# Performance work log

Measured on AMD Instinct MI355X. Metric: run time of the kernel, lower is better.

The kernel has to match this reference:

```python
import jax, jax.numpy as jnp
import numpy as np

N = 50000   # nodes
E = 800000  # edges (avg degree 16)
G = 64      # graphs in batch


def setup_inputs() -> dict:
    key = jax.random.key(0)
    ks = jax.random.split(key, 32)
    w = lambda k, shape, s=0.05: (jax.random.normal(k, shape, jnp.float32) * s)
    inp = {}
    inp["x"] = jax.random.normal(ks[0], (N, 3), jnp.float32)
    inp["edge_index"] = jax.random.randint(ks[1], (2, E), 0, N)
    inp["batch"] = jnp.sort(jax.random.randint(ks[2], (N,), 0, G))
    # TransformerConv 1: in=3, heads=2, d=32 -> out 64 (concat)
    inp["Wq1"] = w(ks[3], (3, 64));  inp["bq1"] = w(ks[4], (64,))
    inp["Wk1"] = w(ks[5], (3, 64));  inp["bk1"] = w(ks[6], (64,))
    inp["Wv1"] = w(ks[7], (3, 64));  inp["bv1"] = w(ks[8], (64,))
    inp["Ws1"] = w(ks[9], (3, 64));  inp["bs1"] = w(ks[10], (64,))
    # TransformerConv 2: in=64, heads=2, d=64 -> out 128 (concat)
    inp["Wq2"] = w(ks[11], (64, 128)); inp["bq2"] = w(ks[12], (128,))
    inp["Wk2"] = w(ks[13], (64, 128)); inp["bk2"] = w(ks[14], (128,))
    inp["Wv2"] = w(ks[15], (64, 128)); inp["bv2"] = w(ks[16], (128,))
    inp["Ws2"] = w(ks[17], (64, 128)); inp["bs2"] = w(ks[18], (128,))
    # MLP head
    inp["W1"] = w(ks[19], (128, 32)); inp["b1"] = w(ks[20], (32,))
    inp["W2"] = w(ks[21], (32, 128)); inp["b2"] = w(ks[22], (128,))
    inp["W3"] = w(ks[23], (128, 40)); inp["b3"] = w(ks[24], (40,))
    return inp


def _transformer_conv(x, src, dst, Wq, bq, Wk, bk, Wv, bv, Ws, bs, H, d):
    """PyG TransformerConv (concat=True, root_weight=True, beta=False)."""
    n = x.shape[0]
    q = (x @ Wq + bq).reshape(n, H, d)
    k = (x @ Wk + bk).reshape(n, H, d)
    v = (x @ Wv + bv).reshape(n, H, d)
    # per-edge attention logits: q_i . k_j / sqrt(d), i=dst, j=src  -> [E, H]
    s = (q[dst] * k[src]).sum(-1) / jnp.sqrt(jnp.float32(d))
    # segment softmax over edges grouped by destination node
    m = jax.ops.segment_max(s, dst, num_segments=n)
    m = jnp.where(jnp.isfinite(m), m, 0.0)
    e = jnp.exp(s - m[dst])
    denom = jax.ops.segment_sum(e, dst, num_segments=n)
    alpha = e / jnp.maximum(denom[dst], 1e-16)
    # scatter-add weighted values
    out = jax.ops.segment_sum(alpha[:, :, None] * v[src], dst, num_segments=n)
    return out.reshape(n, H * d) + x @ Ws + bs  # skip connection


def reference(x, edge_index, batch,
              Wq1, bq1, Wk1, bk1, Wv1, bv1, Ws1, bs1,
              Wq2, bq2, Wk2, bk2, Wv2, bv2, Ws2, bs2,
              W1, b1, W2, b2, W3, b3):
    src, dst = edge_index[0], edge_index[1]
    h = jax.nn.relu(_transformer_conv(x, src, dst, Wq1, bq1, Wk1, bk1,
                                      Wv1, bv1, Ws1, bs1, 2, 32))
    h = jax.nn.relu(_transformer_conv(h, src, dst, Wq2, bq2, Wk2, bk2,
                                      Wv2, bv2, Ws2, bs2, 2, 64))
    # global max pool over graphs
    p = jax.ops.segment_max(h, batch, num_segments=G)
    p = jnp.where(jnp.isfinite(p), p, 0.0)
    x_latent = jax.nn.relu(p @ W1 + b1)
    y = jax.nn.relu(x_latent @ W2 + b2)
    return (y @ W3 + b3, x_latent)
```

## Files before the change

### kernel.cpp

```cpp
#include <hip/hip_runtime.h>
#include <hip/hip_bf16.h>

typedef short s16x8 __attribute__((ext_vector_type(8)));
typedef float f32x4 __attribute__((ext_vector_type(4)));

#define LOG2E 1.4426950408889634f

__device__ __forceinline__ float bfl(unsigned w) { return __uint_as_float(w << 16); }
__device__ __forceinline__ float bfh(unsigned w) { return __uint_as_float(w & 0xffff0000u); }
__device__ __forceinline__ unsigned f2bf(float f) {
    unsigned u = __float_as_uint(f);
    return (u + 0x7fffu + ((u >> 16) & 1u)) >> 16;
}

__global__ void deg_kernel(const int* __restrict__ dst, int* __restrict__ deg, int E) {
    int e = blockIdx.x * blockDim.x + threadIdx.x;
    if (e < E) atomicAdd(&deg[dst[e]], 1);
}

__global__ void scan_reduce(const int* __restrict__ deg, int* __restrict__ bsum, int n) {
    __shared__ int sh[256];
    int t = threadIdx.x;
    int i = blockIdx.x * 256 + t;
    sh[t] = (i < n) ? deg[i] : 0;
    __syncthreads();
    for (int s = 128; s > 0; s >>= 1) {
        if (t < s) sh[t] += sh[t + s];
        __syncthreads();
    }
    if (t == 0) bsum[blockIdx.x] = sh[0];
}

__global__ void scan_blocks(const int* __restrict__ bsum, int* __restrict__ boff,
                            int nb, int* __restrict__ off, int n) {
    __shared__ int sh[256];
    int t = threadIdx.x;
    int v = (t < nb) ? bsum[t] : 0;
    sh[t] = v;
    __syncthreads();
    for (int d = 1; d < 256; d <<= 1) {
        int x = (t >= d) ? sh[t - d] : 0;
        __syncthreads();
        sh[t] += x;
        __syncthreads();
    }
    if (t < nb) boff[t] = sh[t] - v;
    if (t == 255) off[n] = sh[255];
}

__global__ void scan_apply(const int* __restrict__ deg, const int* __restrict__ boff,
                           int* __restrict__ off, int* __restrict__ cursor, int n) {
    __shared__ int sh[256];
    int t = threadIdx.x;
    int i = blockIdx.x * 256 + t;
    int v = (i < n) ? deg[i] : 0;
    sh[t] = v;
    __syncthreads();
    for (int d = 1; d < 256; d <<= 1) {
        int x = (t >= d) ? sh[t - d] : 0;
        __syncthreads();
        sh[t] += x;
        __syncthreads();
    }
    int ex = sh[t] - v + boff[blockIdx.x];
    if (i < n) {
        off[i] = ex;
        cursor[i] = ex;
    }
}

__global__ void scatter_kernel(const int* __restrict__ src, const int* __restrict__ dst,
                               int* __restrict__ cursor, int* __restrict__ srcs, int E) {
    int e = blockIdx.x * blockDim.x + threadIdx.x;
    if (e < E) {
        int p = atomicAdd(&cursor[dst[e]], 1);
        srcs[p] = src[e];
    }
}

__global__ void prep_all(const float* __restrict__ Wq1, const float* __restrict__ bq1,
                         const float* __restrict__ Wk1,
                         const float* __restrict__ Wq2, const float* __restrict__ bq2,
                         const float* __restrict__ Wk2,
                         const float* __restrict__ Wv2, const float* __restrict__ Ws2,
                         float* __restrict__ c1, float* __restrict__ wcat,
                         ushort* __restrict__ bfragY, ushort* __restrict__ B192,
                         int* __restrict__ deg, unsigned* __restrict__ pool,
                         int n, int nbdeg, int poolsz) {
    int b = blockIdx.x, t = threadIdx.x;
    if (b == 0) {
        if (t < 18) {
            int h = t / 9, rr = t % 9, r = rr / 3, rp = rr % 3;
            float s = 0.f;
            for (int d = 0; d < 32; ++d)
                s += Wq1[r * 64 + h * 32 + d] * Wk1[rp * 64 + h * 32 + d];
            c1[t] = s;
        } else if (t < 24) {
            int u = t - 18, h = u / 3, rp = u % 3;
            float s = 0.f;
            for (int d = 0; d < 32; ++d)
                s += bq1[h * 32 + d] * Wk1[rp * 64 + h * 32 + d];
            c1[t] = s;
        } else if (t >= 64 && t < 192) {
            int cc = t - 64, h = cc >> 6, kp = cc & 63;
            float s = 0.f;
            for (int d = 0; d < 64; ++d)
                s += bq2[h * 64 + d] * Wk2[kp * 128 + h * 64 + d];
            wcat[cc] = s;
        }
    } else if (b < 33) {
        int idx = (b - 1) * 256 + t;
        int k = idx >> 7, cc = idx & 127, h = cc >> 6, kp = cc & 63;
        float s = 0.f;
        for (int d = 0; d < 64; ++d)
            s += Wq2[k * 128 + h * 64 + d] * Wk2[kp * 128 + h * 64 + d];
        int frag = ((cc >> 4) << 1) | (k >> 5);
        int l = (cc & 15) | (((k >> 3) & 3) << 4);
        bfragY[(size_t)frag * 512 + l * 8 + (k & 7)] = (ushort)f2bf(s);
    } else if (b < 45) {
        int tt = (b - 33) * 256 + t;
        int frag = tt >> 6, l = tt & 63;
        int ct = frag / 6, ks = frag % 6;
        int c = ct * 16 + (l & 15);
        int kbase = ks * 32 + ((l >> 4) << 3);
#pragma unroll
        for (int e = 0; e < 8; ++e) {
            int k = kbase + e;
            float v;
            if (k < 64) v = (c < 64) ? Wv2[k * 128 + c] : 0.f;
            else if (k < 128) v = (c >= 64) ? Wv2[(k - 64) * 128 + c] : 0.f;
            else v = Ws2[(k - 128) * 128 + c];
            B192[(size_t)frag * 512 + l * 8 + e] = (ushort)f2bf(v);
        }
    } else if (b < 45 + nbdeg) {
        int i = (b - 45) * 256 + t;
        if (i < n) deg[i] = 0;
    } else {
        int i = (b - 45 - nbdeg) * 256 + t;
        if (i < poolsz) pool[i] = 0;
    }
}

__global__ __launch_bounds__(256) void attn1f(
        const float* __restrict__ x, const float* __restrict__ c1,
        const float* __restrict__ Wv, const float* __restrict__ bv,
        const float* __restrict__ Ws, const float* __restrict__ bs,
        const int* __restrict__ off, const int* __restrict__ srcs,
        unsigned* __restrict__ h1b, int n) {
    int lane = threadIdx.x & 63;
    int g = lane >> 3, sl = lane & 7;
    int i = (blockIdx.x * (blockDim.x >> 6) + (threadIdx.x >> 6)) * 8 + g;
    bool act = i < n;
    int ic = act ? i : 0;
    float x0 = x[ic * 3], x1 = x[ic * 3 + 1], x2 = x[ic * 3 + 2];
    float y0[3], y1[3];
#pragma unroll
    for (int rp = 0; rp < 3; ++rp) {
        y0[rp] = x0 * c1[rp] + x1 * c1[3 + rp] + x2 * c1[6 + rp] + c1[18 + rp];
        y1[rp] = x0 * c1[9 + rp] + x1 * c1[12 + rp] + x2 * c1[15 + rp] + c1[21 + rp];
    }
    const float SC = 0.17677669529663688f * LOG2E;
    int e0 = act ? off[ic] : 0, e1 = act ? off[ic + 1] : 0;
    float d0 = 0.f, d1 = 0.f;
    float a0x = 0.f, a0y = 0.f, a0z = 0.f, a1x = 0.f, a1y = 0.f, a1z = 0.f;
    for (int e = e0 + sl; e < e1; e += 8) {
        int j = srcs[e];
        float xj0 = x[j * 3], xj1 = x[j * 3 + 1], xj2 = x[j * 3 + 2];
        float p0 = exp2f((y0[0] * xj0 + y0[1] * xj1 + y0[2] * xj2) * SC);
        float p1 = exp2f((y1[0] * xj0 + y1[1] * xj1 + y1[2] * xj2) * SC);
        d0 += p0; a0x += p0 * xj0; a0y += p0 * xj1; a0z += p0 * xj2;
        d1 += p1; a1x += p1 * xj0; a1y += p1 * xj1; a1z += p1 * xj2;
    }
#pragma unroll
    for (int mask = 1; mask <= 4; mask <<= 1) {
        d0 += __shfl_xor(d0, mask); d1 += __shfl_xor(d1, mask);
        a0x += __shfl_xor(a0x, mask); a0y += __shfl_xor(a0y, mask);
        a0z += __shfl_xor(a0z, mask); a1x += __shfl_xor(a1x, mask);
        a1y += __shfl_xor(a1y, mask); a1z += __shfl_xor(a1z, mask);
    }
    if (!act) return;
    int head = sl >> 2;
    float dh = head ? d1 : d0;
    float inv = 1.f / fmaxf(dh, 1e-16f);
    float sg = dh > 0.f ? 1.f : 0.f;
    float Ax = (head ? a1x : a0x) * inv;
    float Ay = (head ? a1y : a0y) * inv;
    float Az = (head ? a1z : a0z) * inv;
    unsigned pk[4];
#pragma unroll
    for (int u = 0; u < 4; ++u) {
        int c = sl * 8 + 2 * u;
        float2 wv0 = *(const float2*)&Wv[c], wv1 = *(const float2*)&Wv[64 + c],
               wv2 = *(const float2*)&Wv[128 + c];
        float2 ws0 = *(const float2*)&Ws[c], ws1 = *(const float2*)&Ws[64 + c],
               ws2 = *(const float2*)&Ws[128 + c];
        float2 bbv = *(const float2*)&bv[c];
        float2 bbs = *(const float2*)&bs[c];
        float v0 = Ax * wv0.x + Ay * wv1.x + Az * wv2.x + sg * bbv.x +
                   x0 * ws0.x + x1 * ws1.x + x2 * ws2.x + bbs.x;
        float v1 = Ax * wv0.y + Ay * wv1.y + Az * wv2.y + sg * bbv.y +
                   x0 * ws0.y + x1 * ws1.y + x2 * ws2.y + bbs.y;
        pk[u] = f2bf(fmaxf(v0, 0.f)) | (f2bf(fmaxf(v1, 0.f)) << 16);
    }
    uint4 pa = {pk[0], pk[1], pk[2], pk[3]};
    *(uint4*)&h1b[(size_t)i * 32 + sl * 4] = pa;
}

__global__ __launch_bounds__(256) void lin2Y(const ushort* __restrict__ h1b,
                                             const ushort* __restrict__ bfragY,
                                             const float* __restrict__ wcat,
                                             float* __restrict__ Yp, int n) {
    int node0 = blockIdx.x * 16;
    int w = threadIdx.x >> 6, l = threadIdx.x & 63;
    int arow = node0 + (l & 15);
    if (arow >= n) arow = n - 1;
    s16x8 a0 = *(const s16x8*)&h1b[(size_t)arow * 64 + ((l >> 4) << 3)];
    s16x8 a1 = *(const s16x8*)&h1b[(size_t)arow * 64 + 32 + ((l >> 4) << 3)];
    int cl = l & 15;
#pragma unroll
    for (int qq = 0; qq < 2; ++qq) {
        int ct = w * 2 + qq;
        s16x8 b0 = *(const s16x8*)&bfragY[(size_t)(ct * 2 + 0) * 512 + l * 8];
        s16x8 b1 = *(const s16x8*)&bfragY[(size_t)(ct * 2 + 1) * 512 + l * 8];
        f32x4 acc = {0.f, 0.f, 0.f, 0.f};
        acc = __builtin_amdgcn_mfma_f32_16x16x32_bf16(a0, b0, acc, 0, 0, 0);
        acc = __builtin_amdgcn_mfma_f32_16x16x32_bf16(a1, b1, acc, 0, 0, 0);
        int cg = ct * 16 + cl;
        float bb = wcat[cg];
#pragma unroll
        for (int r = 0; r < 4; ++r) {
            int node = node0 + ((l >> 4) << 2) + r;
            if (node < n) Yp[(size_t)node * 128 + cg] = acc[r] + bb;
        }
    }
}

__global__ void attn2_kernel(const float* __restrict__ Yp, const unsigned* __restrict__ h1u,
                             const int* __restrict__ off, const int* __restrict__ srcs,
                             unsigned* __restrict__ a01, float2* __restrict__ sig2, int n) {
    int i = blockIdx.x * (blockDim.x >> 6) + (threadIdx.x >> 6);
    int lane = threadIdx.x & 63;
    if (i >= n) return;
    int og = lane >> 3, sl = lane & 7;
    int e0 = off[i], e1 = off[i + 1];
    const float SC = 0.125f * LOG2E;
    float4 ya0 = *(const float4*)&Yp[(size_t)i * 128 + 8 * sl];
    float4 ya1 = *(const float4*)&Yp[(size_t)i * 128 + 8 * sl + 4];
    float4 yb0 = *(const float4*)&Yp[(size_t)i * 128 + 64 + 8 * sl];
    float4 yb1 = *(const float4*)&Yp[(size_t)i * 128 + 64 + 8 * sl + 4];
    float d0 = 0.f, d1 = 0.f;
    float a0[8] = {0.f, 0.f, 0.f, 0.f, 0.f, 0.f, 0.f, 0.f};
    float a1[8] = {0.f, 0.f, 0.f, 0.f, 0.f, 0.f, 0.f, 0.f};
    for (int e = e0 + og; e < e1; e += 8) {
        int j = srcs[e];
        uint4 hb = *(const uint4*)&h1u[(size_t)j * 32 + 4 * sl];
        float h[8];
        h[0] = bfl(hb.x); h[1] = bfh(hb.x); h[2] = bfl(hb.y); h[3] = bfh(hb.y);
        h[4] = bfl(hb.z); h[5] = bfh(hb.z); h[6] = bfl(hb.w); h[7] = bfh(hb.w);
        float t0 = ya0.x * h[0] + ya0.y * h[1] + ya0.z * h[2] + ya0.w * h[3] +
                   ya1.x * h[4] + ya1.y * h[5] + ya1.z * h[6] + ya1.w * h[7];
        float t1 = yb0.x * h[0] + yb0.y * h[1] + yb0.z * h[2] + yb0.w * h[3] +
                   yb1.x * h[4] + yb1.y * h[5] + yb1.z * h[6] + yb1.w * h[7];
        t0 += __shfl_xor(t0, 1); t0 += __shfl_xor(t0, 2); t0 += __shfl_xor(t0, 4);
        t1 += __shfl_xor(t1, 1); t1 += __shfl_xor(t1, 2); t1 += __shfl_xor(t1, 4);
        float p0 = exp2f(t0 * SC);
        float p1 = exp2f(t1 * SC);
        d0 += p0;
        d1 += p1;
#pragma unroll
        for (int k = 0; k < 8; ++k) {
            a0[k] += p0 * h[k];
            a1[k] += p1 * h[k];
        }
    }
#pragma unroll
    for (int mask = 8; mask <= 32; mask <<= 1) {
        d0 += __shfl_xor(d0, mask);
        d1 += __shfl_xor(d1, mask);
#pragma unroll
        for (int k = 0; k < 8; ++k) {
            a0[k] += __shfl_xor(a0[k], mask);
            a1[k] += __shfl_xor(a1[k], mask);
        }
    }
    if (og == 0) {
        float i0 = 1.f / fmaxf(d0, 1e-16f), i1 = 1.f / fmaxf(d1, 1e-16f);
        uint4 pa, pb;
        pa.x = f2bf(a0[0] * i0) | (f2bf(a0[1] * i0) << 16);
        pa.y = f2bf(a0[2] * i0) | (f2bf(a0[3] * i0) << 16);
        pa.z = f2bf(a0[4] * i0) | (f2bf(a0[5] * i0) << 16);
        pa.w = f2bf(a0[6] * i0) | (f2bf(a0[7] * i0) << 16);
        pb.x = f2bf(a1[0] * i1) | (f2bf(a1[1] * i1) << 16);
        pb.y = f2bf(a1[2] * i1) | (f2bf(a1[3] * i1) << 16);
        pb.z = f2bf(a1[4] * i1) | (f2bf(a1[5] * i1) << 16);
        pb.w = f2bf(a1[6] * i1) | (f2bf(a1[7] * i1) << 16);
        *(uint4*)&a01[(size_t)i * 64 + 4 * sl] = pa;
        *(uint4*)&a01[(size_t)i * 64 + 32 + 4 * sl] = pb;
        if (sl == 0) {
            float2 sg = {d0 > 0.f ? 1.f : 0.f, d1 > 0.f ? 1.f : 0.f};
            sig2[i] = sg;
        }
    }
}

__global__ __launch_bounds__(256) void epi2(
        const ushort* __restrict__ a01, const ushort* __restrict__ h1b,
        const ushort* __restrict__ B192, const float* __restrict__ bv,
        const float* __restrict__ bs, const float* __restrict__ sig2,
        const int* __restrict__ batch, unsigned* __restrict__ pool, int n) {
    __shared__ float po[16][128];
    __shared__ int pg[16];
    int node0 = blockIdx.x * 16;
    int w = threadIdx.x >> 6, l = threadIdx.x & 63;
    int arow = node0 + (l & 15);
    int arc = (arow < n) ? arow : (n - 1);
    int koff = (l >> 4) << 3;
    s16x8 af[6];
    af[0] = *(const s16x8*)&a01[(size_t)arc * 128 + 0 + koff];
    af[1] = *(const s16x8*)&a01[(size_t)arc * 128 + 32 + koff];
    af[2] = *(const s16x8*)&a01[(size_t)arc * 128 + 64 + koff];
    af[3] = *(const s16x8*)&a01[(size_t)arc * 128 + 96 + koff];
    af[4] = *(const s16x8*)&h1b[(size_t)arc * 64 + 0 + koff];
    af[5] = *(const s16x8*)&h1b[(size_t)arc * 64 + 32 + koff];
    if (threadIdx.x < 16)
        pg[threadIdx.x] = (node0 + threadIdx.x < n) ? batch[node0 + threadIdx.x] : -1;
    int cl = l & 15;
#pragma unroll
    for (int qq = 0; qq < 2; ++qq) {
        int ct = w * 2 + qq;
        f32x4 acc = {0.f, 0.f, 0.f, 0.f};
#pragma unroll
        for (int ks = 0; ks < 6; ++ks) {
            s16x8 b = *(const s16x8*)&B192[(size_t)(ct * 6 + ks) * 512 + l * 8];
            acc = __builtin_amdgcn_mfma_f32_16x16x32_bf16(af[ks], b, acc, 0, 0, 0);
        }
        int cg = ct * 16 + cl;
        int head = cg >> 6;
        float bbs = bs[cg], bbv = bv[cg];
#pragma unroll
        for (int r = 0; r < 4; ++r) {
            int row = ((l >> 4) << 2) + r;
            int node = node0 + row;
            float sg = (node < n) ? sig2[node * 2 + head] : 0.f;
            po[row][cg] = fmaxf(acc[r] + sg * bbv + bbs, 0.f);
        }
    }
    __syncthreads();
    int t = threadIdx.x;
    if (t < 128) {
        int curg = -1;
        float mx = 0.f;
        for (int r = 0; r < 16; ++r) {
            int g = pg[r];
            if (g < 0) continue;
            if (g != curg) {
                if (curg >= 0) atomicMax(&pool[(size_t)curg * 128 + t], __float_as_uint(mx));
                curg = g;
                mx = 0.f;
            }
            mx = fmaxf(mx, po[r][t]);
        }
        if (curg >= 0) atomicMax(&pool[(size_t)curg * 128 + t], __float_as_uint(mx));
    }
}

__global__ void head_kernel(const unsigned* __restrict__ pbits,
                            const float* __restrict__ W1, const float* __restrict__ b1,
                            const float* __restrict__ W2, const float* __restrict__ b2,
                            const float* __restrict__ W3, const float* __restrict__ b3,
                            float* __restrict__ out, int G) {
    int g = blockIdx.x;
    int t = threadIdx.x;
    __shared__ float ps[128], xl[32], y[128];
    ps[t] = __uint_as_float(pbits[g * 128 + t]);
    __syncthreads();
    if (t < 32) {
        float a = b1[t];
        for (int k = 0; k < 128; ++k) a += ps[k] * W1[k * 32 + t];
        a = fmaxf(a, 0.f);
        xl[t] = a;
        out[G * 40 + g * 32 + t] = a;
    }
    __syncthreads();
    {
        float a = b2[t];
        for (int k = 0; k < 32; ++k) a += xl[k] * W2[k * 128 + t];
        y[t] = fmaxf(a, 0.f);
    }
    __syncthreads();
    if (t < 40) {
        float a = b3[t];
        for (int k = 0; k < 128; ++k) a += y[k] * W3[k * 40 + t];
        out[g * 40 + t] = a;
    }
}

extern "C" void kernel_launch(void* const* d_in, const int* in_sizes, int n_in,
                              void* d_out, int out_size, void* d_ws, size_t ws_size,
                              hipStream_t stream) {
    const float* x = (const float*)d_in[0];
    const int* eidx = (const int*)d_in[1];
    const int* batch = (const int*)d_in[2];
    const float *Wq1 = (const float*)d_in[3], *bq1 = (const float*)d_in[4];
    const float *Wk1 = (const float*)d_in[5], *bk1 = (const float*)d_in[6];
    const float *Wv1 = (const float*)d_in[7], *bv1 = (const float*)d_in[8];
    const float *Ws1 = (const float*)d_in[9], *bs1 = (const float*)d_in[10];
    const float *Wq2 = (const float*)d_in[11], *bq2 = (const float*)d_in[12];
    const float *Wk2 = (const float*)d_in[13], *bk2 = (const float*)d_in[14];
    const float *Wv2 = (const float*)d_in[15], *bv2 = (const float*)d_in[16];
    const float *Ws2 = (const float*)d_in[17], *bs2 = (const float*)d_in[18];
    const float *W1 = (const float*)d_in[19], *b1 = (const float*)d_in[20];
    const float *W2 = (const float*)d_in[21], *b2 = (const float*)d_in[22];
    const float *W3 = (const float*)d_in[23], *b3 = (const float*)d_in[24];
    (void)bk1; (void)bk2;

    const int N = in_sizes[0] / 3;
    const int E = in_sizes[1] / 2;
    const int G = out_size / 72;
    const int* esrc = eidx;
    const int* edst = eidx + E;
    const int NB = (N + 255) / 256;
    const int POOLSZ = G * 128;
    const int PB = (POOLSZ + 255) / 256;

    char* w = (char*)d_ws;
    size_t o = 0;
    auto alloc = [&](size_t bytes) {
        void* p = w + o;
        o = (o + bytes + 255) & ~(size_t)255;
        return p;
    };
    float* c1buf = (float*)alloc(24 * 4);
    float* wcat = (float*)alloc(128 * 4);
    ushort* bfragY = (ushort*)alloc(16 * 512 * 2);
    ushort* B192 = (ushort*)alloc(48 * 512 * 2);
    unsigned* h1b = (unsigned*)alloc((size_t)N * 32 * 4);
    float* Yp = (float*)alloc((size_t)N * 128 * 4);
    unsigned* a01 = (unsigned*)alloc((size_t)N * 64 * 4);
    float* sig2 = (float*)alloc((size_t)N * 2 * 4);
    int* deg = (int*)alloc((size_t)N * 4);
    int* off = (int*)alloc((size_t)(N + 1) * 4);
    int* cursor = (int*)alloc((size_t)N * 4);
    int* srcs = (int*)alloc((size_t)E * 4);
    unsigned* pool = (unsigned*)alloc((size_t)POOLSZ * 4);
    int* bsum = (int*)alloc(256 * 4);
    int* boff = (int*)alloc(256 * 4);
    (void)ws_size;

    prep_all<<<45 + NB + PB, 256, 0, stream>>>(Wq1, bq1, Wk1, Wq2, bq2, Wk2, Wv2, Ws2,
                                               c1buf, wcat, bfragY, B192, deg, pool,
                                               N, NB, POOLSZ);

    deg_kernel<<<(E + 255) / 256, 256, 0, stream>>>(edst, deg, E);
    scan_reduce<<<NB, 256, 0, stream>>>(deg, bsum, N);
    scan_blocks<<<1, 256, 0, stream>>>(bsum, boff, NB, off, N);
    scan_apply<<<NB, 256, 0, stream>>>(deg, boff, off, cursor, N);
    scatter_kernel<<<(E + 255) / 256, 256, 0, stream>>>(esrc, edst, cursor, srcs, E);

    attn1f<<<(N + 31) / 32, 256, 0, stream>>>(x, c1buf, Wv1, bv1, Ws1, bs1, off, srcs,
                                              h1b, N);

    lin2Y<<<(N + 15) / 16, 256, 0, stream>>>((const ushort*)h1b, bfragY, wcat, Yp, N);
    attn2_kernel<<<(N + 3) / 4, 256, 0, stream>>>(Yp, h1b, off, srcs, a01,
                                                  (float2*)sig2, N);
    epi2<<<(N + 15) / 16, 256, 0, stream>>>((const ushort*)a01, (const ushort*)h1b, B192,
                                            bv2, bs2, sig2, batch, pool, N);

    head_kernel<<<G, 128, 0, stream>>>(pool, W1, b1, W2, b2, W3, b3, (float*)d_out, G);
}
```

Baseline: 193.8 us.

## Split layer-2 attention into score kernel and weighted-aggregation kernel

Splits the fused layer-2 attention kernel in two. The first kernel computes per-edge exponentiated scores and writes them to a new E-sized float2 buffer. The second kernel aggregates, with one wave per node and one feature per lane, looping over edges serially. This removes the 16-accumulator register pressure and the cross-lane reduction tree, but adds an extra kernel launch, a full E*8-byte write and re-read, and a second gather of h1 rows with a serial per-edge loop.

```diff
diff --git a/kernel.cpp b/kernel.cpp
--- a/kernel.cpp
+++ b/kernel.cpp
@@ -8,6 +8,7 @@
 
 __device__ __forceinline__ float bfl(unsigned w) { return __uint_as_float(w << 16); }
 __device__ __forceinline__ float bfh(unsigned w) { return __uint_as_float(w & 0xffff0000u); }
+__device__ __forceinline__ float ubf(ushort u) { return __uint_as_float((unsigned)u << 16); }
 __device__ __forceinline__ unsigned f2bf(float f) {
     unsigned u = __float_as_uint(f);
     return (u + 0x7fffu + ((u >> 16) & 1u)) >> 16;
@@ -235,9 +236,10 @@
     }
 }
 
-__global__ void attn2_kernel(const float* __restrict__ Yp, const unsigned* __restrict__ h1u,
-                             const int* __restrict__ off, const int* __restrict__ srcs,
-                             unsigned* __restrict__ a01, float2* __restrict__ sig2, int n) {
+__global__ __launch_bounds__(256) void attn2s(
+        const float* __restrict__ Yp, const unsigned* __restrict__ h1u,
+        const int* __restrict__ off, const int* __restrict__ srcs,
+        float2* __restrict__ pbuf, int n) {
     int i = blockIdx.x * (blockDim.x >> 6) + (threadIdx.x >> 6);
     int lane = threadIdx.x & 63;
     if (i >= n) return;
@@ -248,58 +250,46 @@
     float4 ya1 = *(const float4*)&Yp[(size_t)i * 128 + 8 * sl + 4];
     float4 yb0 = *(const float4*)&Yp[(size_t)i * 128 + 64 + 8 * sl];
     float4 yb1 = *(const float4*)&Yp[(size_t)i * 128 + 64 + 8 * sl + 4];
-    float d0 = 0.f, d1 = 0.f;
-    float a0[8] = {0.f, 0.f, 0.f, 0.f, 0.f, 0.f, 0.f, 0.f};
-    float a1[8] = {0.f, 0.f, 0.f, 0.f, 0.f, 0.f, 0.f, 0.f};
     for (int e = e0 + og; e < e1; e += 8) {
         int j = srcs[e];
         uint4 hb = *(const uint4*)&h1u[(size_t)j * 32 + 4 * sl];
-        float h[8];
-        h[0] = bfl(hb.x); h[1] = bfh(hb.x); h[2] = bfl(hb.y); h[3] = bfh(hb.y);
-        h[4] = bfl(hb.z); h[5] = bfh(hb.z); h[6] = bfl(hb.w); h[7] = bfh(hb.w);
-        float t0 = ya0.x * h[0] + ya0.y * h[1] + ya0.z * h[2] + ya0.w * h[3] +
-                   ya1.x * h[4] + ya1.y * h[5] + ya1.z * h[6] + ya1.w * h[7];
-        float t1 = yb0.x * h[0] + yb0.y * h[1] + yb0.z * h[2] + yb0.w * h[3] +
-                   yb1.x * h[4] + yb1.y * h[5] + yb1.z * h[6] + yb1.w * h[7];
+        float t0 = ya0.x * bfl(hb.x) + ya0.y * bfh(hb.x) + ya0.z * bfl(hb.y) +
+                   ya0.w * bfh(hb.y) + ya1.x * bfl(hb.z) + ya1.y * bfh(hb.z) +
+                   ya1.z * bfl(hb.w) + ya1.w * bfh(hb.w);
+        float t1 = yb0.x * bfl(hb.x) + yb0.y * bfh(hb.x) + yb0.z * bfl(hb.y) +
+                   yb0.w * bfh(hb.y) + yb1.x * bfl(hb.z) + yb1.y * bfh(hb.z) +
+                   yb1.z * bfl(hb.w) + yb1.w * bfh(hb.w);
         t0 += __shfl_xor(t0, 1); t0 += __shfl_xor(t0, 2); t0 += __shfl_xor(t0, 4);
         t1 += __shfl_xor(t1, 1); t1 += __shfl_xor(t1, 2); t1 += __shfl_xor(t1, 4);
-        float p0 = exp2f(t0 * SC);
-        float p1 = exp2f(t1 * SC);
-        d0 += p0;
-        d1 += p1;
-#pragma unroll
-        for (int k = 0; k < 8; ++k) {
-            a0[k] += p0 * h[k];
-            a1[k] += p1 * h[k];
-        }
-    }
-#pragma unroll
-    for (int mask = 8; mask <= 32; mask <<= 1) {
-        d0 += __shfl_xor(d0, mask);
-        d1 += __shfl_xor(d1, mask);
-#pragma unroll
-        for (int k = 0; k < 8; ++k) {
-            a0[k] += __shfl_xor(a0[k], mask);
-            a1[k] += __shfl_xor(a1[k], mask);
-        }
-    }
-    if (og == 0) {
-        float i0 = 1.f / fmaxf(d0, 1e-16f), i1 = 1.f / fmaxf(d1, 1e-16f);
-        uint4 pa, pb;
-        pa.x = f2bf(a0[0] * i0) | (f2bf(a0[1] * i0) << 16);
-        pa.y = f2bf(a0[2] * i0) | (f2bf(a0[3] * i0) << 16);
-        pa.z = f2bf(a0[4] * i0) | (f2bf(a0[5] * i0) << 16);
-        pa.w = f2bf(a0[6] * i0) | (f2bf(a0[7] * i0) << 16);
-        pb.x = f2bf(a1[0] * i1) | (f2bf(a1[1] * i1) << 16);
-        pb.y = f2bf(a1[2] * i1) | (f2bf(a1[3] * i1) << 16);
-        pb.z = f2bf(a1[4] * i1) | (f2bf(a1[5] * i1) << 16);
-        pb.w = f2bf(a1[6] * i1) | (f2bf(a1[7] * i1) << 16);
-        *(uint4*)&a01[(size_t)i * 64 + 4 * sl] = pa;
-        *(uint4*)&a01[(size_t)i * 64 + 32 + 4 * sl] = pb;
         if (sl == 0) {
-            float2 sg = {d0 > 0.f ? 1.f : 0.f, d1 > 0.f ? 1.f : 0.f};
-            sig2[i] = sg;
-        }
+            float2 p = {exp2f(t0 * SC), exp2f(t1 * SC)};
+            pbuf[e] = p;
+        }
+    }
+}
+
+__global__ __launch_bounds__(256) void attn2pv(
+        const ushort* __restrict__ h1w, const int* __restrict__ off,
+        const int* __restrict__ srcs, const float2* __restrict__ pbuf,
+        ushort* __restrict__ a01, float2* __restrict__ sig2, int n) {
+    int i = blockIdx.x * (blockDim.x >> 6) + (threadIdx.x >> 6);
+    int lane = threadIdx.x & 63;
+    if (i >= n) return;
+    int e0 = off[i], e1 = off[i + 1];
+    float a0 = 0.f, a1 = 0.f, d0 = 0.f, d1 = 0.f;
+    for (int e = e0; e < e1; ++e) {
+        int j = srcs[e];
+        float2 p = pbuf[e];
+        float h = ubf(h1w[(size_t)j * 64 + lane]);
+        a0 += p.x * h; a1 += p.y * h;
+        d0 += p.x; d1 += p.y;
+    }
+    float i0 = 1.f / fmaxf(d0, 1e-16f), i1 = 1.f / fmaxf(d1, 1e-16f);
+    a01[(size_t)i * 128 + lane] = (ushort)f2bf(a0 * i0);
+    a01[(size_t)i * 128 + 64 + lane] = (ushort)f2bf(a1 * i1);
+    if (lane == 0) {
+        float2 sg = {d0 > 0.f ? 1.f : 0.f, d1 > 0.f ? 1.f : 0.f};
+        sig2[i] = sg;
     }
 }
 
@@ -436,8 +426,9 @@
     ushort* B192 = (ushort*)alloc(48 * 512 * 2);
     unsigned* h1b = (unsigned*)alloc((size_t)N * 32 * 4);
     float* Yp = (float*)alloc((size_t)N * 128 * 4);
-    unsigned* a01 = (unsigned*)alloc((size_t)N * 64 * 4);
+    ushort* a01 = (ushort*)alloc((size_t)N * 128 * 2);
     float* sig2 = (float*)alloc((size_t)N * 2 * 4);
+    float2* pbuf = (float2*)alloc((size_t)E * 8);
     int* deg = (int*)alloc((size_t)N * 4);
     int* off = (int*)alloc((size_t)(N + 1) * 4);
     int* cursor = (int*)alloc((size_t)N * 4);
@@ -461,9 +452,10 @@
                                               h1b, N);
 
     lin2Y<<<(N + 15) / 16, 256, 0, stream>>>((const ushort*)h1b, bfragY, wcat, Yp, N);
-    attn2_kernel<<<(N + 3) / 4, 256, 0, stream>>>(Yp, h1b, off, srcs, a01,
-                                                  (float2*)sig2, N);
-    epi2<<<(N + 15) / 16, 256, 0, stream>>>((const ushort*)a01, (const ushort*)h1b, B192,
+    attn2s<<<(N + 3) / 4, 256, 0, stream>>>(Yp, h1b, off, srcs, pbuf, N);
+    attn2pv<<<(N + 3) / 4, 256, 0, stream>>>((const ushort*)h1b, off, srcs, pbuf,
+                                             a01, (float2*)sig2, N);
+    epi2<<<(N + 15) / 16, 256, 0, stream>>>(a01, (const ushort*)h1b, B192,
                                             bv2, bs2, sig2, batch, pool, N);
 
     head_kernel<<<G, 128, 0, stream>>>(pool, W1, b1, W2, b2, W3, b3, (float*)d_out, G);
```

New measurement: 257.8 us. 33.0% more time.
